# Kernel optimization log

Measured on AMD Instinct MI355X. Metric: run time of the kernel, lower is better.

## Reference

```python
import jax, jax.numpy as jnp
import numpy as np

T, B, F = 2048, 2, 1024
H = 16
DK = F // H


def setup_inputs() -> dict:
    key = jax.random.key(0)
    ks = jax.random.split(key, 13)
    s = 0.02
    return {
        "query": jax.random.normal(ks[0], (T, B, F), jnp.float32),
        "key": jax.random.normal(ks[1], (T, B, F), jnp.float32),
        "value": jax.random.normal(ks[2], (T, B, F), jnp.float32),
        "key_padding_mask": jax.random.randint(ks[3], (B, T), 0, 2).astype(bool),
        "Wq": jax.random.normal(ks[4], (F, F), jnp.float32) * s,
        "bq": jnp.zeros((F,), jnp.float32),
        "Wk": jax.random.normal(ks[5], (F, F), jnp.float32) * s,
        "bk": jnp.zeros((F,), jnp.float32),
        "Wv": jax.random.normal(ks[6], (F, F), jnp.float32) * s,
        "bv": jnp.zeros((F,), jnp.float32),
        "Wo": jax.random.normal(ks[7], (F, F), jnp.float32) * s,
        "bo": jnp.zeros((F,), jnp.float32),
    }


def reference(query, key, value, key_padding_mask, Wq, bq, Wk, bk, Wv, bv, Wo, bo):
    # inputs are [T, B, F]; module transposes to batch-major [B, T, F]
    q = jnp.swapaxes(query, 0, 1)
    k = jnp.swapaxes(key, 0, 1)
    v = jnp.swapaxes(value, 0, 1)
    nb = q.shape[0]
    # QKV projections, split into heads: [B, H, T, DK]
    def proj(x, W, b):
        y = x @ W.T + b
        return y.reshape(nb, -1, H, DK).transpose(0, 2, 1, 3)
    qh, kh, vh = proj(q, Wq, bq), proj(k, Wk, bk), proj(v, Wv, bv)
    # scores [B, H, Tq, Tk]
    scores = jnp.einsum("bhqd,bhkd->bhqk", qh, kh) / jnp.sqrt(jnp.float32(DK))
    scores = jnp.where(key_padding_mask[:, None, None, :], -jnp.inf, scores)
    attn = jax.nn.softmax(scores, axis=-1)
    # AV + merge heads + out proj (dropout p=0 -> identity)
    ctx = jnp.einsum("bhqk,bhkd->bhqd", attn, vh)
    ctx = ctx.transpose(0, 2, 1, 3).reshape(nb, -1, H * DK)
    out = ctx @ Wo.T + bo
    return jnp.swapaxes(out, 0, 1)  # back to [T, B, F]
```

## Files before the change

### kernel.cpp

```cpp
#include <hip/hip_runtime.h>
#include <hip/hip_bf16.h>
#include <stdint.h>


typedef __bf16 bf16_t;
typedef __bf16 bf16x4 __attribute__((ext_vector_type(4)));
typedef __bf16 bf16x8 __attribute__((ext_vector_type(8)));
typedef float f32x4 __attribute__((ext_vector_type(4)));
typedef unsigned int u32x2 __attribute__((ext_vector_type(2)));

typedef const __attribute__((address_space(1))) void* gas_ptr;
typedef __attribute__((address_space(3))) void* las_ptr;

__device__ __forceinline__ void gload16(const void* g, void* lds) {
    __builtin_amdgcn_global_load_lds((gas_ptr)g, (las_ptr)lds, 16, 0, 0);
}

__device__ __forceinline__ int swz(int o) { return o ^ (((o >> 7) & 7) << 4); }

__device__ __forceinline__ int gofs(int c) {
    return ((c >> 5) << 9) + (((c >> 1) & 3) << 7) + (((c >> 3) & 3) << 5) + ((c & 1) << 4);
}

#define TRREAD(dst, addr, IMM) \
    asm volatile("ds_read_b64_tr_b16 %0, %1 offset:" #IMM : "=v"(dst) : "v"(addr))

#if __has_builtin(__builtin_amdgcn_exp2f)
#define EXP2F(x) __builtin_amdgcn_exp2f(x)
#else
#define EXP2F(x) exp2f(x)
#endif
#if __has_builtin(__builtin_amdgcn_rcpf)
#define RCPF(x) __builtin_amdgcn_rcpf(x)
#else
#define RCPF(x) (1.0f / (x))
#endif

__global__ __launch_bounds__(256) void prep_all_kernel(const float* __restrict__ wq,
                                                       const float* __restrict__ wk,
                                                       const float* __restrict__ wv,
                                                       const float* __restrict__ wo,
                                                       const unsigned char* __restrict__ mraw,
                                                       bf16_t* __restrict__ wdst,
                                                       unsigned long long* __restrict__ mbits) {
    const int bidx = blockIdx.x;
    const int tid = threadIdx.x;
    if (bidx < 2048) {
        int idx = bidx * 256 + tid;
        int which = idx >> 17;
        int loc = idx & 131071;
        const float* src = which == 0 ? wq : which == 1 ? wk : which == 2 ? wv : wo;
        int e0 = loc * 8;
        const float4* s = (const float4*)(src + e0);
        float4 a = s[0], c = s[1];
        bf16x8 o;
        o[0] = (bf16_t)a.x; o[1] = (bf16_t)a.y; o[2] = (bf16_t)a.z; o[3] = (bf16_t)a.w;
        o[4] = (bf16_t)c.x; o[5] = (bf16_t)c.y; o[6] = (bf16_t)c.z; o[7] = (bf16_t)c.w;
        *(bf16x8*)(wdst + (size_t)which * 1048576 + e0) = o;
    } else {
        __shared__ int s_isbyte;
        if (tid == 0) s_isbyte = 0;
        __syncthreads();
        int any = 0;
        for (int i = tid; i < 4096; i += 256)
            if ((i & 3) && mraw[i]) any = 1;
        if (any) atomicOr(&s_isbyte, 1);
        __syncthreads();
        if (tid < 64) {
            int b = tid >> 5, kt = tid & 31;
            unsigned long long bits = 0;
            if (s_isbyte) {
                for (int j = 0; j < 64; ++j)
                    if (mraw[b * 2048 + kt * 64 + j]) bits |= 1ull << j;
            } else {
                const int* ri = (const int*)mraw;
                for (int j = 0; j < 64; ++j)
                    if (ri[b * 2048 + kt * 64 + j]) bits |= 1ull << j;
            }
            mbits[tid] = bits;
        }
    }
}

__global__ __launch_bounds__(256) void gemm_qkv_kernel(const float* __restrict__ x0,
                                                       const float* __restrict__ x1,
                                                       const float* __restrict__ x2,
                                                       const bf16_t* __restrict__ Bw0,
                                                       const float* __restrict__ b0,
                                                       const float* __restrict__ b1,
                                                       const float* __restrict__ b2,
                                                       const unsigned long long* __restrict__ mbits,
                                                       bf16_t* __restrict__ outb) {
    __shared__ __align__(16) bf16_t Asm[128 * 32];
    __shared__ __align__(16) bf16_t Bsm[64 * 32];
    const int tid = threadIdx.x;
    const int wave = tid >> 6, lane = tid & 63;
    const int g = lane >> 4, lr = lane & 15;

    const int sid = (blockIdx.x & 7) * 192 + (blockIdx.x >> 3);
    const int z = sid >> 9;
    const int rem = sid & 511;
    const int m0 = (rem >> 4) * 128, n0 = (rem & 15) * 64;

    const float* Xf = z == 0 ? x0 : z == 1 ? x1 : x2;
    const bf16_t* Bw = Bw0 + (size_t)z * 1048576;
    const float* bias = z == 0 ? b0 : z == 1 ? b1 : b2;
    const float qsc = (z == 0) ? 0.18033688f : 1.0f;
    const int wm = (wave >> 1) * 64, wn = (wave & 1) * 32;
    const int srow = wave * 32 + (lane >> 2);
    const int scol = (lane & 3) * 8;

    const int r0 = m0 + srow, r1 = r0 + 16;
    const size_t fb0 = (size_t)((r0 & 2047) * 2 + (r0 >> 11)) * 1024 + scol;
    const size_t fb1 = (size_t)((r1 & 2047) * 2 + (r1 >> 11)) * 1024 + scol;
    const bf16_t* gB = Bw + (size_t)(n0 + wave * 16 + (lane >> 2)) * 1024 + scol;
    char* dA0 = (char*)Asm + wave * 2048 + lane * 16;
    char* dA1 = dA0 + 1024;
    char* dB  = (char*)Bsm + wave * 1024;

    f32x4 acc[4][2] = {};
    float4 a00, a01, a10, a11;

    a00 = *(const float4*)(Xf + fb0);
    a01 = *(const float4*)(Xf + fb0 + 4);
    a10 = *(const float4*)(Xf + fb1);
    a11 = *(const float4*)(Xf + fb1 + 4);

    for (int k0 = 0; k0 < 1024; k0 += 32) {
        __syncthreads();
        {
            bf16x8 w0, w1;
            w0[0] = (bf16_t)a00.x; w0[1] = (bf16_t)a00.y; w0[2] = (bf16_t)a00.z; w0[3] = (bf16_t)a00.w;
            w0[4] = (bf16_t)a01.x; w0[5] = (bf16_t)a01.y; w0[6] = (bf16_t)a01.z; w0[7] = (bf16_t)a01.w;
            w1[0] = (bf16_t)a10.x; w1[1] = (bf16_t)a10.y; w1[2] = (bf16_t)a10.z; w1[3] = (bf16_t)a10.w;
            w1[4] = (bf16_t)a11.x; w1[5] = (bf16_t)a11.y; w1[6] = (bf16_t)a11.z; w1[7] = (bf16_t)a11.w;
            *(bf16x8*)dA0 = w0;
            *(bf16x8*)dA1 = w1;
            gload16(gB + k0, dB);
        }
        __syncthreads();

        if (k0 < 992) {
            a00 = *(const float4*)(Xf + fb0 + k0 + 32);
            a01 = *(const float4*)(Xf + fb0 + k0 + 36);
            a10 = *(const float4*)(Xf + fb1 + k0 + 32);
            a11 = *(const float4*)(Xf + fb1 + k0 + 36);
        }

        bf16x8 af[4], bfr[2];
        #pragma unroll
        for (int mi = 0; mi < 4; ++mi)
            af[mi] = *(const bf16x8*)(Asm + (wm + mi * 16 + lr) * 32 + g * 8);
        #pragma unroll
        for (int ni = 0; ni < 2; ++ni)
            bfr[ni] = *(const bf16x8*)(Bsm + (wn + ni * 16 + lr) * 32 + g * 8);
        #pragma unroll
        for (int mi = 0; mi < 4; ++mi)
            #pragma unroll
            for (int ni = 0; ni < 2; ++ni)
                acc[mi][ni] = __builtin_amdgcn_mfma_f32_16x16x32_bf16(af[mi], bfr[ni], acc[mi][ni], 0, 0, 0);
    }

    #pragma unroll
    for (int mi = 0; mi < 4; ++mi) {
        #pragma unroll
        for (int ni = 0; ni < 2; ++ni) {
            int n = n0 + wn + ni * 16 + lr;
            float bs = bias[n];
            #pragma unroll
            for (int i = 0; i < 4; ++i) {
                int m = m0 + wm + mi * 16 + 4 * g + i;
                float v = (acc[mi][ni][i] + bs) * qsc;
                int b = m >> 11, t = m & 2047;
                if (z != 0) {
                    const bool mk = (mbits[b * 32 + (t >> 6)] >> (t & 63)) & 1;
                    if (mk) v = 0.f;
                }
                int hh = n >> 6, dk = n & 63;
                outb[(size_t)z * 4194304 + ((size_t)(b * 16 + hh) * 2048 + t) * 64 + dk] = (bf16_t)v;
            }
        }
    }
}

__global__ __launch_bounds__(256) void gemm_out_kernel(const bf16_t* __restrict__ Ab,
                                                       const bf16_t* __restrict__ Bw,
                                                       const float* __restrict__ bias,
                                                       float* __restrict__ outf) {
    __shared__ __align__(16) bf16_t Asm[128 * 32];
    __shared__ __align__(16) bf16_t Bsm[128 * 32];
    const int tid = threadIdx.x;
    const int wave = tid >> 6, lane = tid & 63;
    const int g = lane >> 4, lr = lane & 15;

    const int sid = (blockIdx.x & 7) * 32 + (blockIdx.x >> 3);
    const int m0 = (sid >> 3) * 128, n0 = (sid & 7) * 128;
    const int wm = (wave >> 1) * 64, wn = (wave & 1) * 64;
    const int srow = wave * 32 + (lane >> 2);
    const int scol = (lane & 3) * 8;
    const int r0 = m0 + srow, r1 = r0 + 16;

    f32x4 acc[4][4] = {};

    for (int k0 = 0; k0 < 1024; k0 += 32) {
        __syncthreads();
        gload16(Ab + (size_t)r0 * 1024 + k0 + scol,               (char*)Asm + wave * 2048);
        gload16(Ab + (size_t)r1 * 1024 + k0 + scol,               (char*)Asm + wave * 2048 + 1024);
        gload16(Bw + (size_t)(n0 + srow) * 1024 + k0 + scol,      (char*)Bsm + wave * 2048);
        gload16(Bw + (size_t)(n0 + srow + 16) * 1024 + k0 + scol, (char*)Bsm + wave * 2048 + 1024);
        __syncthreads();

        bf16x8 af[4], bfr[4];
        #pragma unroll
        for (int mi = 0; mi < 4; ++mi)
            af[mi] = *(const bf16x8*)(Asm + (wm + mi * 16 + lr) * 32 + g * 8);
        #pragma unroll
        for (int ni = 0; ni < 4; ++ni)
            bfr[ni] = *(const bf16x8*)(Bsm + (wn + ni * 16 + lr) * 32 + g * 8);
        #pragma unroll
        for (int mi = 0; mi < 4; ++mi)
            #pragma unroll
            for (int ni = 0; ni < 4; ++ni)
                acc[mi][ni] = __builtin_amdgcn_mfma_f32_16x16x32_bf16(af[mi], bfr[ni], acc[mi][ni], 0, 0, 0);
    }

    #pragma unroll
    for (int mi = 0; mi < 4; ++mi) {
        #pragma unroll
        for (int ni = 0; ni < 4; ++ni) {
            int n = n0 + wn + ni * 16 + lr;
            float bs = bias[n];
            #pragma unroll
            for (int i = 0; i < 4; ++i) {
                int m = m0 + wm + mi * 16 + 4 * g + i;
                int b = m >> 11, t = m & 2047;
                outf[(size_t)t * 2048 + b * 1024 + n] = acc[mi][ni][i] + bs;
            }
        }
    }
}

__global__ __launch_bounds__(256, 2) void attn_kernel(const bf16_t* __restrict__ qh,
                                                      const bf16_t* __restrict__ kh,
                                                      const bf16_t* __restrict__ vh,
                                                      const unsigned long long* __restrict__ mbits,
                                                      bf16_t* __restrict__ ctx) {
    __shared__ __align__(16) bf16_t Ks[2][2][64 * 64];
    __shared__ __align__(16) bf16_t Vs[2][2][64 * 64];

    const int tid = threadIdx.x;
    const int wave = tid >> 6, lane = tid & 63;
    const int g = lane >> 4, lr = lane & 15;
    const int bid = blockIdx.x;
    const int sid = (bid & 7) * 64 + (bid >> 3);
    const int bh = sid >> 4, qc = sid & 15;
    const int b = bh >> 4, h = bh & 15;
    const int q0 = qc * 128;
    const bf16_t* Qg = qh + ((size_t)bh * 2048 + q0) * 64;
    const bf16_t* Kg = kh + (size_t)bh * 2048 * 64;
    const bf16_t* Vg = vh + (size_t)bh * 2048 * 64;
    const unsigned long long* mbp = mbits + b * 32;

    const int dstw = wave * 2048;
    const int dl = dstw + lane * 16;
    const int wq0 = wave * 32;
    const int vs0 = gofs(wave * 128 + lane);
    const int vs1 = gofs(wave * 128 + 64 + lane);

    #pragma unroll
    for (int c = 0; c < 4; ++c)
        gload16((const char*)Qg + swz(wave * 4096 + c * 1024 + lane * 16),
                (char*)Ks[0] + wave * 4096 + c * 1024);
    __syncthreads();
    bf16x8 qf[2][2];
    #pragma unroll
    for (int s = 0; s < 2; ++s) {
        qf[s][0] = *(const bf16x8*)((const char*)Ks[0] + swz((wq0 + s * 16 + lr) * 128 + g * 16));
        qf[s][1] = *(const bf16x8*)((const char*)Ks[0] + swz((wq0 + s * 16 + lr) * 128 + 64 + g * 16));
    }
    __syncthreads();

    #pragma unroll
    for (int u = 0; u < 2; ++u) {
        const char* Kt = (const char*)(Kg + u * 4096);
        const char* Vt = (const char*)(Vg + u * 4096);
        gload16(Kt + swz(dl),        (char*)Ks[0][u] + dstw);
        gload16(Kt + swz(dl + 1024), (char*)Ks[0][u] + dstw + 1024);
        gload16(Vt + vs0,            (char*)Vs[0][u] + dstw);
        gload16(Vt + vs1,            (char*)Vs[0][u] + dstw + 1024);
    }

    bf16x8 ones;
    #pragma unroll
    for (int j = 0; j < 8; ++j) ones[j] = (bf16_t)1.0f;

    f32x4 cacc[2][4] = {};
    f32x4 sacc[2] = {};
    const unsigned vbase = (unsigned)(unsigned long long)(las_ptr)&Vs[0][0][0] + g * 512 + lr * 8;

    for (int m = 0; m < 16; ++m) {
        const int par = m & 1;
        __syncthreads();

        if (m < 15) {
            #pragma unroll
            for (int u = 0; u < 2; ++u) {
                const char* Kn = (const char*)(Kg + (2 * m + 2 + u) * 4096);
                const char* Vn = (const char*)(Vg + (2 * m + 2 + u) * 4096);
                gload16(Kn + swz(dl),        (char*)Ks[par ^ 1][u] + dstw);
                gload16(Kn + swz(dl + 1024), (char*)Ks[par ^ 1][u] + dstw + 1024);
                gload16(Vn + vs0,            (char*)Vs[par ^ 1][u] + dstw);
                gload16(Vn + vs1,            (char*)Vs[par ^ 1][u] + dstw + 1024);
            }
        }

        f32x4 s2[2][2][4];
        __builtin_amdgcn_s_setprio(1);
        #pragma unroll
        for (int u = 0; u < 2; ++u) {
            const char* Kc = (const char*)Ks[par][u];
            #pragma unroll
            for (int st = 0; st < 4; ++st) {
                bf16x8 kf0 = *(const bf16x8*)(Kc + swz((st * 16 + lr) * 128 + g * 16));
                bf16x8 kf1 = *(const bf16x8*)(Kc + swz((st * 16 + lr) * 128 + 64 + g * 16));
                #pragma unroll
                for (int s = 0; s < 2; ++s) {
                    f32x4 zz = {};
                    zz = __builtin_amdgcn_mfma_f32_16x16x32_bf16(kf0, qf[s][0], zz, 0, 0, 0);
                    zz = __builtin_amdgcn_mfma_f32_16x16x32_bf16(kf1, qf[s][1], zz, 0, 0, 0);
                    s2[u][s][st] = zz;
                }
            }
        }
        __builtin_amdgcn_s_setprio(0);

        #pragma unroll
        for (int u = 0; u < 2; ++u) {
            #pragma unroll
            for (int st = 0; st < 4; ++st) {
                #pragma unroll
                for (int i = 0; i < 4; ++i) {
                    s2[u][0][st][i] = EXP2F(s2[u][0][st][i]);
                    s2[u][1][st][i] = EXP2F(s2[u][1][st][i]);
                }
            }
            bf16x8 pb[2][2];
            #pragma unroll
            for (int s = 0; s < 2; ++s)
                #pragma unroll
                for (int kk = 0; kk < 2; ++kk)
                    #pragma unroll
                    for (int j = 0; j < 8; ++j)
                        pb[s][kk][j] = (bf16_t)s2[u][s][2 * kk + (j >> 2)][j & 3];

            const unsigned vb = vbase + (unsigned)par * 16384u + (unsigned)u * 8192u;
            u32x2 t[2][2][4];
            TRREAD(t[0][0][0], vb, 0);    TRREAD(t[0][0][1], vb, 128);
            TRREAD(t[0][0][2], vb, 256);  TRREAD(t[0][0][3], vb, 384);
            TRREAD(t[0][1][0], vb, 2048); TRREAD(t[0][1][1], vb, 2176);
            TRREAD(t[0][1][2], vb, 2304); TRREAD(t[0][1][3], vb, 2432);
            TRREAD(t[1][0][0], vb, 4096); TRREAD(t[1][0][1], vb, 4224);
            TRREAD(t[1][0][2], vb, 4352); TRREAD(t[1][0][3], vb, 4480);
            TRREAD(t[1][1][0], vb, 6144); TRREAD(t[1][1][1], vb, 6272);
            TRREAD(t[1][1][2], vb, 6400); TRREAD(t[1][1][3], vb, 6528);
            asm volatile("s_waitcnt lgkmcnt(0)" ::: "memory");
            __builtin_amdgcn_sched_barrier(0);
            __builtin_amdgcn_s_setprio(1);
            #pragma unroll
            for (int kk = 0; kk < 2; ++kk) {
                sacc[0] = __builtin_amdgcn_mfma_f32_16x16x32_bf16(ones, pb[0][kk], sacc[0], 0, 0, 0);
                sacc[1] = __builtin_amdgcn_mfma_f32_16x16x32_bf16(ones, pb[1][kk], sacc[1], 0, 0, 0);
                #pragma unroll
                for (int ni = 0; ni < 4; ++ni) {
                    union { u32x2 q[2]; bf16x8 v8; } uu;
                    uu.q[0] = t[kk][0][ni];
                    uu.q[1] = t[kk][1][ni];
                    #pragma unroll
                    for (int s = 0; s < 2; ++s)
                        cacc[s][ni] = __builtin_amdgcn_mfma_f32_16x16x32_bf16(uu.v8, pb[s][kk], cacc[s][ni], 0, 0, 0);
                }
            }
            __builtin_amdgcn_s_setprio(0);
        }
    }

    float nm = 0.f;
    #pragma unroll
    for (int i = 0; i < 32; ++i)
        nm += (float)__popcll(mbp[i]);
    #pragma unroll
    for (int s = 0; s < 2; ++s) {
        const float rl = RCPF(sacc[s][0] - nm);
        const int trow = q0 + wq0 + s * 16 + lr;
        #pragma unroll
        for (int ni = 0; ni < 4; ++ni) {
            bf16x4 o;
            #pragma unroll
            for (int i = 0; i < 4; ++i)
                o[i] = (bf16_t)(cacc[s][ni][i] * rl);
            *(bf16x4*)(ctx + ((size_t)b * 2048 + trow) * 1024 + h * 64 + ni * 16 + 4 * g) = o;
        }
    }
}

extern "C" void kernel_launch(void* const* d_in, const int* in_sizes, int n_in,
                              void* d_out, int out_size, void* d_ws, size_t ws_size,
                              hipStream_t stream) {
    const float* query = (const float*)d_in[0];
    const float* key_  = (const float*)d_in[1];
    const float* value = (const float*)d_in[2];
    const unsigned char* kpm_raw = (const unsigned char*)d_in[3];
    const float* Wq = (const float*)d_in[4];
    const float* bq = (const float*)d_in[5];
    const float* Wk = (const float*)d_in[6];
    const float* bk = (const float*)d_in[7];
    const float* Wv = (const float*)d_in[8];
    const float* bv = (const float*)d_in[9];
    const float* Wo = (const float*)d_in[10];
    const float* bo = (const float*)d_in[11];
    float* out = (float*)d_out;

    char* ws = (char*)d_ws;
    size_t off = 0;
    auto alloc = [&](size_t bytes) {
        char* p = ws + off;
        off += (bytes + 255) & ~(size_t)255;
        return p;
    };
    const size_t SZ_X = (size_t)4096 * 1024 * sizeof(bf16_t);
    const size_t SZ_W = (size_t)1024 * 1024 * sizeof(bf16_t);
    bf16_t* wqb = (bf16_t*)alloc(SZ_W);
    bf16_t* wkb = (bf16_t*)alloc(SZ_W);
    bf16_t* wvb = (bf16_t*)alloc(SZ_W);
    bf16_t* wob = (bf16_t*)alloc(SZ_W);
    bf16_t* qhB = (bf16_t*)alloc(SZ_X);
    bf16_t* khB = (bf16_t*)alloc(SZ_X);
    bf16_t* vhB = (bf16_t*)alloc(SZ_X);
    bf16_t* ctxB = (bf16_t*)alloc(SZ_X);
    unsigned long long* mbits = (unsigned long long*)alloc(64 * sizeof(unsigned long long));
    (void)wkb; (void)wvb;

    prep_all_kernel<<<2049, 256, 0, stream>>>(Wq, Wk, Wv, Wo, kpm_raw, wqb, mbits);

    gemm_qkv_kernel<<<1536, 256, 0, stream>>>(query, key_, value, wqb,
                                              bq, bk, bv, mbits, qhB);

    attn_kernel<<<512, 256, 0, stream>>>(qhB, khB, vhB, mbits, ctxB);

    gemm_out_kernel<<<256, 256, 0, stream>>>(ctxB, wob, bo, out);
}
```

Before: 137.4 us.

## Widen QKV GEMM tile to 128x128 and stage fp32 A via direct LDS loads

The QKV projection GEMM now uses a 128x128 output tile, so each block covers twice the N width and the grid shrinks from 1536 to 768 blocks. The fp32 activation tile is copied straight into shared memory with global_load_lds using a swizzled layout. It is converted to bf16 when fragments are read, which replaces the register prefetch and convert-then-store path. This is meant to improve operand reuse and cut register-staged load traffic, but it doubles the A tile's LDS footprint, loses the explicit register prefetch overlap, and adds conversion work on every fragment read.

```diff
diff --git a/kernel.cpp b/kernel.cpp
--- a/kernel.cpp
+++ b/kernel.cpp
@@ -91,80 +91,74 @@
                                                        const float* __restrict__ b2,
                                                        const unsigned long long* __restrict__ mbits,
                                                        bf16_t* __restrict__ outb) {
-    __shared__ __align__(16) bf16_t Asm[128 * 32];
-    __shared__ __align__(16) bf16_t Bsm[64 * 32];
+    __shared__ __align__(16) float  AsmF[128 * 32];
+    __shared__ __align__(16) bf16_t Bsm[128 * 32];
     const int tid = threadIdx.x;
     const int wave = tid >> 6, lane = tid & 63;
     const int g = lane >> 4, lr = lane & 15;
 
-    const int sid = (blockIdx.x & 7) * 192 + (blockIdx.x >> 3);
-    const int z = sid >> 9;
-    const int rem = sid & 511;
-    const int m0 = (rem >> 4) * 128, n0 = (rem & 15) * 64;
+    const int sid = (blockIdx.x & 7) * 96 + (blockIdx.x >> 3);
+    const int z = sid >> 8;
+    const int rem = sid & 255;
+    const int m0 = (rem >> 3) * 128, n0 = (rem & 7) * 128;
 
     const float* Xf = z == 0 ? x0 : z == 1 ? x1 : x2;
     const bf16_t* Bw = Bw0 + (size_t)z * 1048576;
     const float* bias = z == 0 ? b0 : z == 1 ? b1 : b2;
     const float qsc = (z == 0) ? 0.18033688f : 1.0f;
-    const int wm = (wave >> 1) * 64, wn = (wave & 1) * 32;
+    const int wm = (wave >> 1) * 64, wn = (wave & 1) * 64;
     const int srow = wave * 32 + (lane >> 2);
     const int scol = (lane & 3) * 8;
 
-    const int r0 = m0 + srow, r1 = r0 + 16;
-    const size_t fb0 = (size_t)((r0 & 2047) * 2 + (r0 >> 11)) * 1024 + scol;
-    const size_t fb1 = (size_t)((r1 & 2047) * 2 + (r1 >> 11)) * 1024 + scol;
-    const bf16_t* gB = Bw + (size_t)(n0 + wave * 16 + (lane >> 2)) * 1024 + scol;
-    char* dA0 = (char*)Asm + wave * 2048 + lane * 16;
-    char* dA1 = dA0 + 1024;
-    char* dB  = (char*)Bsm + wave * 1024;
-
-    f32x4 acc[4][2] = {};
-    float4 a00, a01, a10, a11;
-
-    a00 = *(const float4*)(Xf + fb0);
-    a01 = *(const float4*)(Xf + fb0 + 4);
-    a10 = *(const float4*)(Xf + fb1);
-    a11 = *(const float4*)(Xf + fb1 + 4);
+    int arow[4], acol[4];
+    #pragma unroll
+    for (int c = 0; c < 4; ++c) {
+        int d = wave * 4096 + c * 1024 + lane * 16;
+        int o = swz(d);
+        int r = m0 + (o >> 7);
+        arow[c] = (r & 2047) * 2 + (r >> 11);
+        acol[c] = (o & 127) >> 2;
+    }
+
+    f32x4 acc[4][4] = {};
 
     for (int k0 = 0; k0 < 1024; k0 += 32) {
         __syncthreads();
-        {
-            bf16x8 w0, w1;
-            w0[0] = (bf16_t)a00.x; w0[1] = (bf16_t)a00.y; w0[2] = (bf16_t)a00.z; w0[3] = (bf16_t)a00.w;
-            w0[4] = (bf16_t)a01.x; w0[5] = (bf16_t)a01.y; w0[6] = (bf16_t)a01.z; w0[7] = (bf16_t)a01.w;
-            w1[0] = (bf16_t)a10.x; w1[1] = (bf16_t)a10.y; w1[2] = (bf16_t)a10.z; w1[3] = (bf16_t)a10.w;
-            w1[4] = (bf16_t)a11.x; w1[5] = (bf16_t)a11.y; w1[6] = (bf16_t)a11.z; w1[7] = (bf16_t)a11.w;
-            *(bf16x8*)dA0 = w0;
-            *(bf16x8*)dA1 = w1;
-            gload16(gB + k0, dB);
-        }
-        __syncthreads();
-
-        if (k0 < 992) {
-            a00 = *(const float4*)(Xf + fb0 + k0 + 32);
-            a01 = *(const float4*)(Xf + fb0 + k0 + 36);
-            a10 = *(const float4*)(Xf + fb1 + k0 + 32);
-            a11 = *(const float4*)(Xf + fb1 + k0 + 36);
-        }
-
-        bf16x8 af[4], bfr[2];
+        #pragma unroll
+        for (int c = 0; c < 4; ++c)
+            gload16(Xf + (size_t)arow[c] * 1024 + k0 + acol[c],
+                    (char*)AsmF + wave * 4096 + c * 1024);
+        gload16(Bw + (size_t)(n0 + srow) * 1024 + k0 + scol,      (char*)Bsm + wave * 2048);
+        gload16(Bw + (size_t)(n0 + srow + 16) * 1024 + k0 + scol, (char*)Bsm + wave * 2048 + 1024);
+        __syncthreads();
+
+        bf16x8 af[4], bfr[4];
+        #pragma unroll
+        for (int mi = 0; mi < 4; ++mi) {
+            const int row = wm + mi * 16 + lr;
+            const int base = row * 128 + g * 32;
+            const int sw = (row & 7) << 4;
+            float4 lo = *(const float4*)((const char*)AsmF + (base ^ sw));
+            float4 hi = *(const float4*)((const char*)AsmF + ((base + 16) ^ sw));
+            af[mi][0] = (bf16_t)lo.x; af[mi][1] = (bf16_t)lo.y;
+            af[mi][2] = (bf16_t)lo.z; af[mi][3] = (bf16_t)lo.w;
+            af[mi][4] = (bf16_t)hi.x; af[mi][5] = (bf16_t)hi.y;
+            af[mi][6] = (bf16_t)hi.z; af[mi][7] = (bf16_t)hi.w;
+        }
+        #pragma unroll
+        for (int ni = 0; ni < 4; ++ni)
+            bfr[ni] = *(const bf16x8*)(Bsm + (wn + ni * 16 + lr) * 32 + g * 8);
         #pragma unroll
         for (int mi = 0; mi < 4; ++mi)
-            af[mi] = *(const bf16x8*)(Asm + (wm + mi * 16 + lr) * 32 + g * 8);
-        #pragma unroll
-        for (int ni = 0; ni < 2; ++ni)
-            bfr[ni] = *(const bf16x8*)(Bsm + (wn + ni * 16 + lr) * 32 + g * 8);
-        #pragma unroll
-        for (int mi = 0; mi < 4; ++mi)
-            #pragma unroll
-            for (int ni = 0; ni < 2; ++ni)
+            #pragma unroll
+            for (int ni = 0; ni < 4; ++ni)
                 acc[mi][ni] = __builtin_amdgcn_mfma_f32_16x16x32_bf16(af[mi], bfr[ni], acc[mi][ni], 0, 0, 0);
     }
 
     #pragma unroll
     for (int mi = 0; mi < 4; ++mi) {
         #pragma unroll
-        for (int ni = 0; ni < 2; ++ni) {
+        for (int ni = 0; ni < 4; ++ni) {
             int n = n0 + wn + ni * 16 + lr;
             float bs = bias[n];
             #pragma unroll
@@ -442,8 +436,8 @@
 
     prep_all_kernel<<<2049, 256, 0, stream>>>(Wq, Wk, Wv, Wo, kpm_raw, wqb, mbits);
 
-    gemm_qkv_kernel<<<1536, 256, 0, stream>>>(query, key_, value, wqb,
-                                              bq, bk, bv, mbits, qhB);
+    gemm_qkv_kernel<<<768, 256, 0, stream>>>(query, key_, value, wqb,
+                                             bq, bk, bv, mbits, qhB);
 
     attn_kernel<<<512, 256, 0, stream>>>(qhB, khB, vhB, mbits, ctxB);
 
```

Result: faster. 127.9 us (-6.9%).

## Widen QKV GEMM tile to 128x128 with 4-stage async B-tile prefetch

Applied to the files above, without the earlier changes.

The QKV projection GEMM now uses 128x128 output tiles instead of 128x64, which halves the grid and doubles the MFMA work per wave relative to the A-tile loads. Weight tiles are streamed into a 4-slot LDS ring with global_load_lds issued two iterations ahead. The __syncthreads pairs are replaced by raw s_barrier plus an explicit lgkmcnt wait. The aim is more data reuse per block and load latency hidden behind compute. In exchange it uses more LDS and accumulator registers, and it relies on implicit vmcnt waits from the A loads to guarantee the async B data has landed.

```diff
diff --git a/kernel.cpp b/kernel.cpp
--- a/kernel.cpp
+++ b/kernel.cpp
@@ -92,42 +92,48 @@
                                                        const unsigned long long* __restrict__ mbits,
                                                        bf16_t* __restrict__ outb) {
     __shared__ __align__(16) bf16_t Asm[128 * 32];
-    __shared__ __align__(16) bf16_t Bsm[64 * 32];
+    __shared__ __align__(16) bf16_t Bsm[4][128 * 32];
     const int tid = threadIdx.x;
     const int wave = tid >> 6, lane = tid & 63;
     const int g = lane >> 4, lr = lane & 15;
 
-    const int sid = (blockIdx.x & 7) * 192 + (blockIdx.x >> 3);
-    const int z = sid >> 9;
-    const int rem = sid & 511;
-    const int m0 = (rem >> 4) * 128, n0 = (rem & 15) * 64;
+    const int sid = (blockIdx.x & 7) * 96 + (blockIdx.x >> 3);
+    const int z = sid >> 8;
+    const int rem = sid & 255;
+    const int m0 = (rem >> 3) * 128, n0 = (rem & 7) * 128;
 
     const float* Xf = z == 0 ? x0 : z == 1 ? x1 : x2;
     const bf16_t* Bw = Bw0 + (size_t)z * 1048576;
     const float* bias = z == 0 ? b0 : z == 1 ? b1 : b2;
     const float qsc = (z == 0) ? 0.18033688f : 1.0f;
-    const int wm = (wave >> 1) * 64, wn = (wave & 1) * 32;
+    const int wm = (wave >> 1) * 64, wn = (wave & 1) * 64;
     const int srow = wave * 32 + (lane >> 2);
     const int scol = (lane & 3) * 8;
 
     const int r0 = m0 + srow, r1 = r0 + 16;
     const size_t fb0 = (size_t)((r0 & 2047) * 2 + (r0 >> 11)) * 1024 + scol;
     const size_t fb1 = (size_t)((r1 & 2047) * 2 + (r1 >> 11)) * 1024 + scol;
-    const bf16_t* gB = Bw + (size_t)(n0 + wave * 16 + (lane >> 2)) * 1024 + scol;
+    const bf16_t* gB0 = Bw + (size_t)(n0 + srow) * 1024 + scol;
+    const bf16_t* gB1 = Bw + (size_t)(n0 + srow + 16) * 1024 + scol;
     char* dA0 = (char*)Asm + wave * 2048 + lane * 16;
     char* dA1 = dA0 + 1024;
-    char* dB  = (char*)Bsm + wave * 1024;
-
-    f32x4 acc[4][2] = {};
+
+    f32x4 acc[4][4] = {};
     float4 a00, a01, a10, a11;
 
+    gload16(gB0,      (char*)Bsm[0] + wave * 2048);
+    gload16(gB1,      (char*)Bsm[0] + wave * 2048 + 1024);
     a00 = *(const float4*)(Xf + fb0);
     a01 = *(const float4*)(Xf + fb0 + 4);
     a10 = *(const float4*)(Xf + fb1);
     a11 = *(const float4*)(Xf + fb1 + 4);
-
-    for (int k0 = 0; k0 < 1024; k0 += 32) {
-        __syncthreads();
+    gload16(gB0 + 32, (char*)Bsm[1] + wave * 2048);
+    gload16(gB1 + 32, (char*)Bsm[1] + wave * 2048 + 1024);
+
+    for (int it = 0; it < 32; ++it) {
+        const int k0 = it * 32;
+        __builtin_amdgcn_s_barrier();
+        __builtin_amdgcn_sched_barrier(0);
         {
             bf16x8 w0, w1;
             w0[0] = (bf16_t)a00.x; w0[1] = (bf16_t)a00.y; w0[2] = (bf16_t)a00.z; w0[3] = (bf16_t)a00.w;
@@ -136,35 +142,40 @@
             w1[4] = (bf16_t)a11.x; w1[5] = (bf16_t)a11.y; w1[6] = (bf16_t)a11.z; w1[7] = (bf16_t)a11.w;
             *(bf16x8*)dA0 = w0;
             *(bf16x8*)dA1 = w1;
-            gload16(gB + k0, dB);
-        }
-        __syncthreads();
-
-        if (k0 < 992) {
+        }
+        if (it < 31) {
             a00 = *(const float4*)(Xf + fb0 + k0 + 32);
             a01 = *(const float4*)(Xf + fb0 + k0 + 36);
             a10 = *(const float4*)(Xf + fb1 + k0 + 32);
             a11 = *(const float4*)(Xf + fb1 + k0 + 36);
         }
-
-        bf16x8 af[4], bfr[2];
+        if (it < 30) {
+            gload16(gB0 + k0 + 64, (char*)Bsm[(it + 2) & 3] + wave * 2048);
+            gload16(gB1 + k0 + 64, (char*)Bsm[(it + 2) & 3] + wave * 2048 + 1024);
+        }
+        asm volatile("s_waitcnt lgkmcnt(0)" ::: "memory");
+        __builtin_amdgcn_s_barrier();
+        __builtin_amdgcn_sched_barrier(0);
+
+        const bf16_t* Bc = Bsm[it & 3];
+        bf16x8 af[4], bfr[4];
         #pragma unroll
         for (int mi = 0; mi < 4; ++mi)
             af[mi] = *(const bf16x8*)(Asm + (wm + mi * 16 + lr) * 32 + g * 8);
         #pragma unroll
-        for (int ni = 0; ni < 2; ++ni)
-            bfr[ni] = *(const bf16x8*)(Bsm + (wn + ni * 16 + lr) * 32 + g * 8);
+        for (int ni = 0; ni < 4; ++ni)
+            bfr[ni] = *(const bf16x8*)(Bc + (wn + ni * 16 + lr) * 32 + g * 8);
         #pragma unroll
         for (int mi = 0; mi < 4; ++mi)
             #pragma unroll
-            for (int ni = 0; ni < 2; ++ni)
+            for (int ni = 0; ni < 4; ++ni)
                 acc[mi][ni] = __builtin_amdgcn_mfma_f32_16x16x32_bf16(af[mi], bfr[ni], acc[mi][ni], 0, 0, 0);
     }
 
     #pragma unroll
     for (int mi = 0; mi < 4; ++mi) {
         #pragma unroll
-        for (int ni = 0; ni < 2; ++ni) {
+        for (int ni = 0; ni < 4; ++ni) {
             int n = n0 + wn + ni * 16 + lr;
             float bs = bias[n];
             #pragma unroll
@@ -442,8 +453,8 @@
 
     prep_all_kernel<<<2049, 256, 0, stream>>>(Wq, Wk, Wv, Wo, kpm_raw, wqb, mbits);
 
-    gemm_qkv_kernel<<<1536, 256, 0, stream>>>(query, key_, value, wqb,
-                                              bq, bk, bv, mbits, qhB);
+    gemm_qkv_kernel<<<768, 256, 0, stream>>>(query, key_, value, wqb,
+                                             bq, bk, bv, mbits, qhB);
 
     attn_kernel<<<512, 256, 0, stream>>>(qhB, khB, vhB, mbits, ctxB);
 
```

After: 122.6 us (median of 3 runs). 10.7% less time.
